# Kernel tuning notes

Measured on AMD Instinct MI355X. Metric: run time of the kernel, lower is better.

The kernel has to match this reference:

```python
import jax, jax.numpy as jnp
import numpy as np

DEPTH = 4  # default MLP(dim, depth=4) in NeuralMemory.__init__


def mlp_apply(W, x):
    # MLP.forward: x @ W0, then silu(x) @ Wi for i>0
    for i in range(DEPTH):
        if i:
            x = jax.nn.silu(x)
        x = x @ W[i]
    return x


def _loss(W, k, v):
    # default_loss_fn on a single token: (pred - target)^2 .mean(-1).sum() == mean over d
    pred = mlp_apply(W, k)
    return ((pred - v) ** 2).mean()


def setup_inputs() -> dict:
    key = jax.random.key(0)
    ks = jax.random.split(key, 6)
    b, n, d = 2, 1024, 128
    s = 1.0 / np.sqrt(d)  # scale weights for numerical sanity through the 4-layer chain
    return {
        "seq": jax.random.normal(ks[0], (b, n, d), dtype=jnp.float32),
        "W": jax.random.normal(ks[1], (DEPTH, d, d), dtype=jnp.float32) * s,
        "Wkv": jax.random.normal(ks[2], (d, 2 * d), dtype=jnp.float32) * s,
        "w_lr": jax.random.normal(ks[3], (d,), dtype=jnp.float32) * s,
        "w_mom": jax.random.normal(ks[4], (d,), dtype=jnp.float32) * s,
        "w_decay": jax.random.normal(ks[5], (d,), dtype=jnp.float32) * s,
    }


def reference(seq, W, Wkv, w_lr, w_mom, w_decay):
    # NeuralMemory.store_memories (past_memories=None)
    b, n, d = seq.shape
    adaptive_lr = seq @ w_lr                     # (b, n)  -- to_adaptive_step (no activation)
    adaptive_momentum = seq @ w_mom              # (b, n)  -- computed but unused in source snippet
    decay_factor = jax.nn.sigmoid(seq @ w_decay) # (b, n)  -- computed but unused in source snippet

    flat = seq.reshape(b * n, d)
    kv = flat @ Wkv
    keys, values = kv[:, :d], kv[:, d:]

    # per-sample grad_and_value over flattened tokens
    per_sample = jax.vmap(jax.value_and_grad(_loss), in_axes=(None, 0, 0))
    losses, grads = per_sample(W, keys, values)  # losses (b*n,), grads (b*n, DEPTH, d, d)

    grads = grads.reshape(b, n, DEPTH, d, d)
    grads = grads * (-adaptive_lr)[:, :, None, None, None]
    grads = jnp.cumsum(grads, axis=1)            # fast-weight cumulative updates

    next_memories = W[None] + grads[:, -1]       # (b, DEPTH, d, d)
    return grads, next_memories, losses.mean()
```

## Files before the change

kernel.cpp:

```cpp
#include <hip/hip_runtime.h>
#include <math.h>

#define D 128
#define NS 2048
#define NCHUNK 16
#define CLEN 64

__device__ __forceinline__ float sigmoidf_(float x) {
    return 1.0f / (1.0f + expf(-x));
}

__device__ __forceinline__ float matvec_col(const float* __restrict__ M,
                                            const float* x, int tid)
{
    float a0 = 0.f, a1 = 0.f, a2 = 0.f, a3 = 0.f;
#pragma unroll 4
    for (int r = 0; r < D; r += 4) {
        a0 += x[r]     * M[(r)     * D + tid];
        a1 += x[r + 1] * M[(r + 1) * D + tid];
        a2 += x[r + 2] * M[(r + 2) * D + tid];
        a3 += x[r + 3] * M[(r + 3) * D + tid];
    }
    return (a0 + a1) + (a2 + a3);
}

__global__ __launch_bounds__(256) void transposeW(
    const float* __restrict__ W, float* __restrict__ WT)
{
    const int l   = blockIdx.x >> 4;
    const int tl  = blockIdx.x & 15;
    const int tr  = tl >> 2, tc = tl & 3;
    const int tid = threadIdx.x;
    const int lr  = tid >> 5;
    const int lc  = tid & 31;
    __shared__ float tile[32][33];
#pragma unroll
    for (int k = 0; k < 4; ++k)
        tile[lr + 8 * k][lc] =
            W[l * 16384 + (tr * 32 + lr + 8 * k) * 128 + tc * 32 + lc];
    __syncthreads();
#pragma unroll
    for (int k = 0; k < 4; ++k)
        WT[l * 16384 + (tc * 32 + lr + 8 * k) * 128 + tr * 32 + lc] =
            tile[lc][lr + 8 * k];
}

__global__ __launch_bounds__(128) void phase1(
    const float* __restrict__ seq, const float* __restrict__ W,
    const float* __restrict__ WT, const float* __restrict__ Wkv,
    const float* __restrict__ w_lr,
    float* __restrict__ ws_u, float* __restrict__ ws_g,
    float* __restrict__ lossbuf)
{
    const int s   = blockIdx.x;
    const int tid = threadIdx.x;

    __shared__ float sseq[D], xbuf[D], vbuf[D], gbuf[D];
    __shared__ float red2[2];

    const float sv = seq[s * D + tid];
    sseq[tid] = sv;

    float p = sv * w_lr[tid];
#pragma unroll
    for (int off = 32; off > 0; off >>= 1) p += __shfl_down(p, off, 64);
    if ((tid & 63) == 0) red2[tid >> 6] = p;
    __syncthreads();
    const float scale = -(red2[0] + red2[1]);

    {
        float k0 = 0.f, k1 = 0.f, v0 = 0.f, v1 = 0.f;
#pragma unroll 4
        for (int r = 0; r < D; r += 2) {
            float x0 = sseq[r], x1 = sseq[r + 1];
            k0 += x0 * Wkv[r * 256 + tid];
            v0 += x0 * Wkv[r * 256 + 128 + tid];
            k1 += x1 * Wkv[(r + 1) * 256 + tid];
            v1 += x1 * Wkv[(r + 1) * 256 + 128 + tid];
        }
        float kacc = k0 + k1, vacc = v0 + v1;
        xbuf[tid] = kacc;
        vbuf[tid] = vacc;
        ws_u[(s * 4 + 0) * D + tid] = kacc;
    }
    __syncthreads();

    float h0r, h1r, h2r;
    {
        float h = matvec_col(W + 0 * 16384, xbuf, tid);
        h0r = h;
        float a = h * sigmoidf_(h);
        __syncthreads();
        xbuf[tid] = a;
        ws_u[(s * 4 + 1) * D + tid] = a;
        __syncthreads();
    }
    {
        float h = matvec_col(W + 1 * 16384, xbuf, tid);
        h1r = h;
        float a = h * sigmoidf_(h);
        __syncthreads();
        xbuf[tid] = a;
        ws_u[(s * 4 + 2) * D + tid] = a;
        __syncthreads();
    }
    {
        float h = matvec_col(W + 2 * 16384, xbuf, tid);
        h2r = h;
        float a = h * sigmoidf_(h);
        __syncthreads();
        xbuf[tid] = a;
        ws_u[(s * 4 + 3) * D + tid] = a;
        __syncthreads();
    }
    const float hfin = matvec_col(W + 3 * 16384, xbuf, tid);
    const float diff = hfin - vbuf[tid];

    {
        float lp = diff * diff;
#pragma unroll
        for (int off = 32; off > 0; off >>= 1) lp += __shfl_down(lp, off, 64);
        if ((tid & 63) == 0) red2[tid >> 6] = lp;
        __syncthreads();
        if (tid == 0) lossbuf[s] = (red2[0] + red2[1]) * (1.0f / 128.0f);
    }

    float g = diff * (2.0f / 128.0f);
    gbuf[tid] = g;
    ws_g[(s * 4 + 3) * D + tid] = scale * g;
    __syncthreads();

    {
        float da = matvec_col(WT + 3 * 16384, gbuf, tid);
        float sg = sigmoidf_(h2r);
        g = da * (sg * (1.0f + h2r * (1.0f - sg)));
    }
    __syncthreads();
    gbuf[tid] = g;
    ws_g[(s * 4 + 2) * D + tid] = scale * g;
    __syncthreads();

    {
        float da = matvec_col(WT + 2 * 16384, gbuf, tid);
        float sg = sigmoidf_(h1r);
        g = da * (sg * (1.0f + h1r * (1.0f - sg)));
    }
    __syncthreads();
    gbuf[tid] = g;
    ws_g[(s * 4 + 1) * D + tid] = scale * g;
    __syncthreads();

    {
        float da = matvec_col(WT + 1 * 16384, gbuf, tid);
        float sg = sigmoidf_(h0r);
        g = da * (sg * (1.0f + h0r * (1.0f - sg)));
    }
    ws_g[(s * 4 + 0) * D + tid] = scale * g;
}

__global__ __launch_bounds__(256) void phaseA(
    const float* __restrict__ ws_u, const float* __restrict__ ws_g,
    float* __restrict__ chunkS)
{
    const int bx    = blockIdx.x;
    const int half  = bx & 1;
    const int cs    = bx >> 1;
    const int j     = cs & 15;
    const int layer = (cs >> 4) & 3;
    const int b     = cs >> 6;
    const int tid   = threadIdx.x;
    const int hi    = tid >> 7;
    const int c     = tid & 127;

    __shared__ float us[2][64], gs[2][D];
    float acc[32];
#pragma unroll
    for (int k = 0; k < 32; ++k) acc[k] = 0.f;

    const int samp0 = b * 1024 + j * CLEN;
    float ru = 0.f, rg = 0.f;
    if (tid < 128) rg = ws_g[(samp0 * 4 + layer) * D + tid];
    if (tid < 64)  ru = ws_u[(samp0 * 4 + layer) * D + half * 64 + tid];

    for (int t = 0; t < CLEN; ++t) {
        const int pb = t & 1;
        if (tid < 128) gs[pb][tid] = rg;
        if (tid < 64)  us[pb][tid] = ru;
        if (t + 1 < CLEN) {
            const int samp = samp0 + t + 1;
            if (tid < 128) rg = ws_g[(samp * 4 + layer) * D + tid];
            if (tid < 64)  ru = ws_u[(samp * 4 + layer) * D + half * 64 + tid];
        }
        __syncthreads();
        const float gv = gs[pb][c];
#pragma unroll
        for (int k = 0; k < 32; ++k) acc[k] += us[pb][2 * k + hi] * gv;
    }
    float* out = chunkS + (size_t)cs * 16384 + half * 8192;
#pragma unroll
    for (int k = 0; k < 32; ++k) out[k * 256 + tid] = acc[k];
}

__global__ __launch_bounds__(256) void phaseA2(float* __restrict__ chunkS)
{
    const int g  = blockIdx.x * 256 + threadIdx.x;
    const int bl = g >> 14;
    const int e  = g & 16383;
    float* base = chunkS + (size_t)bl * NCHUNK * 16384 + e;
    float run = 0.f;
    for (int j = 0; j < NCHUNK; ++j) {
        float t = base[(size_t)j * 16384];
        base[(size_t)j * 16384] = run;
        run += t;
    }
}

__global__ __launch_bounds__(256) void phaseB(
    const float* __restrict__ ws_u, const float* __restrict__ ws_g,
    const float* __restrict__ chunkS, const float* __restrict__ W,
    float* __restrict__ out_grads, float* __restrict__ out_next)
{
    const int id    = blockIdx.x;
    const int rt    = id & 3;
    const int j     = (id >> 2) & 15;
    const int layer = (id >> 6) & 3;
    const int b     = id >> 8;
    const int cs    = (b * 4 + layer) * NCHUNK + j;
    const int tid   = threadIdx.x;

    const int c4 = (tid & 31) * 4;
    const int rq = tid >> 5;
    const int r0 = rt * 32 + rq * 4;

    float4 acc[4];
    const float* carry = chunkS + (size_t)cs * 16384;
#pragma unroll
    for (int k = 0; k < 4; ++k)
        acc[k] = *(const float4*)(carry + (r0 + k) * 128 + c4);

    const int samp0 = b * 1024 + j * CLEN;
    const float* gbase = ws_g + ((size_t)samp0 * 4 + layer) * D;
    const float* ubase = ws_u + ((size_t)samp0 * 4 + layer) * D;

    float4 gv = *(const float4*)(gbase + c4);
    float4 u4 = *(const float4*)(ubase + r0);

    for (int t = 0; t < CLEN; ++t) {
        float4 gn = gv, un = u4;
        if (t + 1 < CLEN) {
            gn = *(const float4*)(gbase + (t + 1) * 512 + c4);
            un = *(const float4*)(ubase + (t + 1) * 512 + r0);
        }
        float* obase = out_grads + ((size_t)(samp0 + t) * 4 + layer) * 16384;

        acc[0].x += u4.x * gv.x; acc[0].y += u4.x * gv.y;
        acc[0].z += u4.x * gv.z; acc[0].w += u4.x * gv.w;
        acc[1].x += u4.y * gv.x; acc[1].y += u4.y * gv.y;
        acc[1].z += u4.y * gv.z; acc[1].w += u4.y * gv.w;
        acc[2].x += u4.z * gv.x; acc[2].y += u4.z * gv.y;
        acc[2].z += u4.z * gv.z; acc[2].w += u4.z * gv.w;
        acc[3].x += u4.w * gv.x; acc[3].y += u4.w * gv.y;
        acc[3].z += u4.w * gv.z; acc[3].w += u4.w * gv.w;

        *(float4*)(obase + (r0 + 0) * 128 + c4) = acc[0];
        *(float4*)(obase + (r0 + 1) * 128 + c4) = acc[1];
        *(float4*)(obase + (r0 + 2) * 128 + c4) = acc[2];
        *(float4*)(obase + (r0 + 3) * 128 + c4) = acc[3];

        gv = gn; u4 = un;
    }

    if (j == NCHUNK - 1) {
#pragma unroll
        for (int k = 0; k < 4; ++k) {
            const int r = r0 + k;
            float4 w4 = *(const float4*)(W + layer * 16384 + r * 128 + c4);
            float4 o;
            o.x = acc[k].x + w4.x;
            o.y = acc[k].y + w4.y;
            o.z = acc[k].z + w4.z;
            o.w = acc[k].w + w4.w;
            *(float4*)(out_next + ((size_t)(b * 4 + layer)) * 16384 + r * 128 + c4) = o;
        }
    }
}

__global__ __launch_bounds__(256) void lossk(const float* __restrict__ lossbuf,
                                             float* __restrict__ out)
{
    __shared__ float red[256];
    const int tid = threadIdx.x;
    float s = 0.f;
    for (int i = tid; i < NS; i += 256) s += lossbuf[i];
    red[tid] = s;
    __syncthreads();
    for (int off = 128; off > 0; off >>= 1) {
        if (tid < off) red[tid] += red[tid + off];
        __syncthreads();
    }
    if (tid == 0) out[0] = red[0] * (1.0f / (float)NS);
}

extern "C" void kernel_launch(void* const* d_in, const int* in_sizes, int n_in,
                              void* d_out, int out_size, void* d_ws, size_t ws_size,
                              hipStream_t stream)
{
    const float* seq   = (const float*)d_in[0];
    const float* W     = (const float*)d_in[1];
    const float* Wkv   = (const float*)d_in[2];
    const float* w_lr  = (const float*)d_in[3];

    float* out = (float*)d_out;
    float* ws  = (float*)d_ws;

    float* ws_u    = ws;
    float* ws_g    = ws + 1048576;
    float* chunkS  = ws + 2097152;
    float* lossbuf = ws + 4194304;
    float* WT      = chunkS;

    float* out_grads = out;
    float* out_next  = out + 134217728;
    float* out_loss  = out + 134348800;

    transposeW<<<64, 256, 0, stream>>>(W, WT);
    phase1<<<NS, 128, 0, stream>>>(seq, W, WT, Wkv, w_lr, ws_u, ws_g, lossbuf);
    phaseA<<<256, 256, 0, stream>>>(ws_u, ws_g, chunkS);
    phaseA2<<<512, 256, 0, stream>>>(chunkS);
    phaseB<<<512, 256, 0, stream>>>(ws_u, ws_g, chunkS, W, out_grads, out_next);
    lossk<<<1, 256, 0, stream>>>(lossbuf, out_loss);
}
```

Measured before the change: 628.5 us.

## Batch four samples per matvec in phase1, finer chunking, nontemporal grad stores

phase1 now has each 128-thread group process four samples at once, so every weight element loaded from global memory is reused across four matvecs, and blocks hold 8 samples. The cumsum chunking doubles to 32 chunks of 32 when the workspace is large enough, giving phaseB 1024 blocks for more parallelism. The 512 MB gradient output is written with nontemporal stores to avoid polluting cache. Risks are higher register pressure in phase1 and a dependence on the available workspace size.

After: 624.8 us. Within noise of the previous version (-0.6%).

```diff
diff --git a/kernel.cpp b/kernel.cpp
--- a/kernel.cpp
+++ b/kernel.cpp
@@ -3,25 +3,33 @@
 
 #define D 128
 #define NS 2048
-#define NCHUNK 16
-#define CLEN 64
+
+typedef float v4f __attribute__((ext_vector_type(4)));
 
 __device__ __forceinline__ float sigmoidf_(float x) {
     return 1.0f / (1.0f + expf(-x));
 }
 
-__device__ __forceinline__ float matvec_col(const float* __restrict__ M,
-                                            const float* x, int tid)
-{
-    float a0 = 0.f, a1 = 0.f, a2 = 0.f, a3 = 0.f;
-#pragma unroll 4
+__device__ __forceinline__ void matvec4(const float* __restrict__ M,
+                                        const float (*xsg)[D], int lt,
+                                        float acc[4])
+{
+    acc[0] = 0.f; acc[1] = 0.f; acc[2] = 0.f; acc[3] = 0.f;
+#pragma unroll 2
     for (int r = 0; r < D; r += 4) {
-        a0 += x[r]     * M[(r)     * D + tid];
-        a1 += x[r + 1] * M[(r + 1) * D + tid];
-        a2 += x[r + 2] * M[(r + 2) * D + tid];
-        a3 += x[r + 3] * M[(r + 3) * D + tid];
-    }
-    return (a0 + a1) + (a2 + a3);
+        v4f x0 = *(const v4f*)&xsg[0][r];
+        v4f x1 = *(const v4f*)&xsg[1][r];
+        v4f x2 = *(const v4f*)&xsg[2][r];
+        v4f x3 = *(const v4f*)&xsg[3][r];
+#pragma unroll
+        for (int rr = 0; rr < 4; ++rr) {
+            float w = M[(r + rr) * D + lt];
+            acc[0] += x0[rr] * w;
+            acc[1] += x1[rr] * w;
+            acc[2] += x2[rr] * w;
+            acc[3] += x3[rr] * w;
+        }
+    }
 }
 
 __global__ __launch_bounds__(256) void transposeW(
@@ -45,119 +53,161 @@
             tile[lc][lr + 8 * k];
 }
 
-__global__ __launch_bounds__(128) void phase1(
+__global__ __launch_bounds__(256) void phase1(
     const float* __restrict__ seq, const float* __restrict__ W,
     const float* __restrict__ WT, const float* __restrict__ Wkv,
     const float* __restrict__ w_lr,
     float* __restrict__ ws_u, float* __restrict__ ws_g,
     float* __restrict__ lossbuf)
 {
-    const int s   = blockIdx.x;
     const int tid = threadIdx.x;
-
-    __shared__ float sseq[D], xbuf[D], vbuf[D], gbuf[D];
-    __shared__ float red2[2];
-
-    const float sv = seq[s * D + tid];
-    sseq[tid] = sv;
-
-    float p = sv * w_lr[tid];
-#pragma unroll
-    for (int off = 32; off > 0; off >>= 1) p += __shfl_down(p, off, 64);
-    if ((tid & 63) == 0) red2[tid >> 6] = p;
-    __syncthreads();
-    const float scale = -(red2[0] + red2[1]);
-
-    {
-        float k0 = 0.f, k1 = 0.f, v0 = 0.f, v1 = 0.f;
-#pragma unroll 4
-        for (int r = 0; r < D; r += 2) {
-            float x0 = sseq[r], x1 = sseq[r + 1];
-            k0 += x0 * Wkv[r * 256 + tid];
-            v0 += x0 * Wkv[r * 256 + 128 + tid];
-            k1 += x1 * Wkv[(r + 1) * 256 + tid];
-            v1 += x1 * Wkv[(r + 1) * 256 + 128 + tid];
-        }
-        float kacc = k0 + k1, vacc = v0 + v1;
-        xbuf[tid] = kacc;
-        vbuf[tid] = vacc;
-        ws_u[(s * 4 + 0) * D + tid] = kacc;
-    }
-    __syncthreads();
-
-    float h0r, h1r, h2r;
-    {
-        float h = matvec_col(W + 0 * 16384, xbuf, tid);
-        h0r = h;
-        float a = h * sigmoidf_(h);
-        __syncthreads();
-        xbuf[tid] = a;
-        ws_u[(s * 4 + 1) * D + tid] = a;
-        __syncthreads();
-    }
-    {
-        float h = matvec_col(W + 1 * 16384, xbuf, tid);
-        h1r = h;
-        float a = h * sigmoidf_(h);
-        __syncthreads();
-        xbuf[tid] = a;
-        ws_u[(s * 4 + 2) * D + tid] = a;
-        __syncthreads();
-    }
-    {
-        float h = matvec_col(W + 2 * 16384, xbuf, tid);
-        h2r = h;
-        float a = h * sigmoidf_(h);
-        __syncthreads();
-        xbuf[tid] = a;
-        ws_u[(s * 4 + 3) * D + tid] = a;
-        __syncthreads();
-    }
-    const float hfin = matvec_col(W + 3 * 16384, xbuf, tid);
-    const float diff = hfin - vbuf[tid];
-
-    {
-        float lp = diff * diff;
+    const int g   = tid >> 7;
+    const int lt  = tid & 127;
+    const int wv  = lt >> 6;
+    const int sbase = blockIdx.x * 8 + g * 4;
+
+    __shared__ float sseq[2][4][D];
+    __shared__ float xs[2][4][D];
+    __shared__ float red[2][4][2];
+
+#pragma unroll
+    for (int s = 0; s < 4; ++s)
+        sseq[g][s][lt] = seq[(sbase + s) * D + lt];
+
+    const float wlr = w_lr[lt];
+#pragma unroll
+    for (int s = 0; s < 4; ++s) {
+        float p = sseq[g][s][lt] * wlr;
+#pragma unroll
+        for (int off = 32; off > 0; off >>= 1) p += __shfl_down(p, off, 64);
+        if ((tid & 63) == 0) red[g][s][wv] = p;
+    }
+    __syncthreads();
+    float sc[4];
+#pragma unroll
+    for (int s = 0; s < 4; ++s) sc[s] = -(red[g][s][0] + red[g][s][1]);
+
+    float ka[4] = {0.f, 0.f, 0.f, 0.f}, va[4] = {0.f, 0.f, 0.f, 0.f};
+#pragma unroll 2
+    for (int r = 0; r < D; r += 4) {
+        v4f x0 = *(const v4f*)&sseq[g][0][r];
+        v4f x1 = *(const v4f*)&sseq[g][1][r];
+        v4f x2 = *(const v4f*)&sseq[g][2][r];
+        v4f x3 = *(const v4f*)&sseq[g][3][r];
+#pragma unroll
+        for (int rr = 0; rr < 4; ++rr) {
+            float wk  = Wkv[(r + rr) * 256 + lt];
+            float wv2 = Wkv[(r + rr) * 256 + 128 + lt];
+            ka[0] += x0[rr] * wk;  va[0] += x0[rr] * wv2;
+            ka[1] += x1[rr] * wk;  va[1] += x1[rr] * wv2;
+            ka[2] += x2[rr] * wk;  va[2] += x2[rr] * wv2;
+            ka[3] += x3[rr] * wk;  va[3] += x3[rr] * wv2;
+        }
+    }
+    float vr[4];
+#pragma unroll
+    for (int s = 0; s < 4; ++s) {
+        vr[s] = va[s];
+        xs[g][s][lt] = ka[s];
+        ws_u[((size_t)(sbase + s) * 4 + 0) * D + lt] = ka[s];
+    }
+    __syncthreads();
+
+    float h0r[4], h1r[4], h2r[4], acc[4];
+
+    matvec4(W + 0 * 16384, xs[g], lt, acc);
+    __syncthreads();
+#pragma unroll
+    for (int s = 0; s < 4; ++s) {
+        h0r[s] = acc[s];
+        float a = acc[s] * sigmoidf_(acc[s]);
+        xs[g][s][lt] = a;
+        ws_u[((size_t)(sbase + s) * 4 + 1) * D + lt] = a;
+    }
+    __syncthreads();
+
+    matvec4(W + 1 * 16384, xs[g], lt, acc);
+    __syncthreads();
+#pragma unroll
+    for (int s = 0; s < 4; ++s) {
+        h1r[s] = acc[s];
+        float a = acc[s] * sigmoidf_(acc[s]);
+        xs[g][s][lt] = a;
+        ws_u[((size_t)(sbase + s) * 4 + 2) * D + lt] = a;
+    }
+    __syncthreads();
+
+    matvec4(W + 2 * 16384, xs[g], lt, acc);
+    __syncthreads();
+#pragma unroll
+    for (int s = 0; s < 4; ++s) {
+        h2r[s] = acc[s];
+        float a = acc[s] * sigmoidf_(acc[s]);
+        xs[g][s][lt] = a;
+        ws_u[((size_t)(sbase + s) * 4 + 3) * D + lt] = a;
+    }
+    __syncthreads();
+
+    matvec4(W + 3 * 16384, xs[g], lt, acc);
+    float diff[4];
+#pragma unroll
+    for (int s = 0; s < 4; ++s) diff[s] = acc[s] - vr[s];
+
+#pragma unroll
+    for (int s = 0; s < 4; ++s) {
+        float lp = diff[s] * diff[s];
 #pragma unroll
         for (int off = 32; off > 0; off >>= 1) lp += __shfl_down(lp, off, 64);
-        if ((tid & 63) == 0) red2[tid >> 6] = lp;
-        __syncthreads();
-        if (tid == 0) lossbuf[s] = (red2[0] + red2[1]) * (1.0f / 128.0f);
-    }
-
-    float g = diff * (2.0f / 128.0f);
-    gbuf[tid] = g;
-    ws_g[(s * 4 + 3) * D + tid] = scale * g;
-    __syncthreads();
-
-    {
-        float da = matvec_col(WT + 3 * 16384, gbuf, tid);
-        float sg = sigmoidf_(h2r);
-        g = da * (sg * (1.0f + h2r * (1.0f - sg)));
-    }
-    __syncthreads();
-    gbuf[tid] = g;
-    ws_g[(s * 4 + 2) * D + tid] = scale * g;
-    __syncthreads();
-
-    {
-        float da = matvec_col(WT + 2 * 16384, gbuf, tid);
-        float sg = sigmoidf_(h1r);
-        g = da * (sg * (1.0f + h1r * (1.0f - sg)));
-    }
-    __syncthreads();
-    gbuf[tid] = g;
-    ws_g[(s * 4 + 1) * D + tid] = scale * g;
-    __syncthreads();
-
-    {
-        float da = matvec_col(WT + 1 * 16384, gbuf, tid);
-        float sg = sigmoidf_(h0r);
-        g = da * (sg * (1.0f + h0r * (1.0f - sg)));
-    }
-    ws_g[(s * 4 + 0) * D + tid] = scale * g;
-}
-
+        if ((tid & 63) == 0) red[g][s][wv] = lp;
+    }
+    __syncthreads();
+    if (lt == 0) {
+#pragma unroll
+        for (int s = 0; s < 4; ++s)
+            lossbuf[sbase + s] = (red[g][s][0] + red[g][s][1]) * (1.0f / 128.0f);
+    }
+
+    float gcur[4];
+#pragma unroll
+    for (int s = 0; s < 4; ++s) {
+        gcur[s] = diff[s] * (2.0f / 128.0f);
+        xs[g][s][lt] = gcur[s];
+        ws_g[((size_t)(sbase + s) * 4 + 3) * D + lt] = sc[s] * gcur[s];
+    }
+    __syncthreads();
+
+    matvec4(WT + 3 * 16384, xs[g], lt, acc);
+    __syncthreads();
+#pragma unroll
+    for (int s = 0; s < 4; ++s) {
+        float hv = h2r[s], sg = sigmoidf_(hv);
+        gcur[s] = acc[s] * (sg * (1.0f + hv * (1.0f - sg)));
+        xs[g][s][lt] = gcur[s];
+        ws_g[((size_t)(sbase + s) * 4 + 2) * D + lt] = sc[s] * gcur[s];
+    }
+    __syncthreads();
+
+    matvec4(WT + 2 * 16384, xs[g], lt, acc);
+    __syncthreads();
+#pragma unroll
+    for (int s = 0; s < 4; ++s) {
+        float hv = h1r[s], sg = sigmoidf_(hv);
+        gcur[s] = acc[s] * (sg * (1.0f + hv * (1.0f - sg)));
+        xs[g][s][lt] = gcur[s];
+        ws_g[((size_t)(sbase + s) * 4 + 1) * D + lt] = sc[s] * gcur[s];
+    }
+    __syncthreads();
+
+    matvec4(WT + 1 * 16384, xs[g], lt, acc);
+#pragma unroll
+    for (int s = 0; s < 4; ++s) {
+        float hv = h0r[s], sg = sigmoidf_(hv);
+        gcur[s] = acc[s] * (sg * (1.0f + hv * (1.0f - sg)));
+        ws_g[((size_t)(sbase + s) * 4 + 0) * D + lt] = sc[s] * gcur[s];
+    }
+}
+
+template<int NCH, int CL>
 __global__ __launch_bounds__(256) void phaseA(
     const float* __restrict__ ws_u, const float* __restrict__ ws_g,
     float* __restrict__ chunkS)
@@ -165,9 +215,9 @@
     const int bx    = blockIdx.x;
     const int half  = bx & 1;
     const int cs    = bx >> 1;
-    const int j     = cs & 15;
-    const int layer = (cs >> 4) & 3;
-    const int b     = cs >> 6;
+    const int j     = cs & (NCH - 1);
+    const int layer = (cs / NCH) & 3;
+    const int b     = cs / (NCH * 4);
     const int tid   = threadIdx.x;
     const int hi    = tid >> 7;
     const int c     = tid & 127;
@@ -177,16 +227,16 @@
 #pragma unroll
     for (int k = 0; k < 32; ++k) acc[k] = 0.f;
 
-    const int samp0 = b * 1024 + j * CLEN;
+    const int samp0 = b * 1024 + j * CL;
     float ru = 0.f, rg = 0.f;
     if (tid < 128) rg = ws_g[(samp0 * 4 + layer) * D + tid];
     if (tid < 64)  ru = ws_u[(samp0 * 4 + layer) * D + half * 64 + tid];
 
-    for (int t = 0; t < CLEN; ++t) {
+    for (int t = 0; t < CL; ++t) {
         const int pb = t & 1;
         if (tid < 128) gs[pb][tid] = rg;
         if (tid < 64)  us[pb][tid] = ru;
-        if (t + 1 < CLEN) {
+        if (t + 1 < CL) {
             const int samp = samp0 + t + 1;
             if (tid < 128) rg = ws_g[(samp * 4 + layer) * D + tid];
             if (tid < 64)  ru = ws_u[(samp * 4 + layer) * D + half * 64 + tid];
@@ -201,20 +251,22 @@
     for (int k = 0; k < 32; ++k) out[k * 256 + tid] = acc[k];
 }
 
+template<int NCH>
 __global__ __launch_bounds__(256) void phaseA2(float* __restrict__ chunkS)
 {
     const int g  = blockIdx.x * 256 + threadIdx.x;
     const int bl = g >> 14;
     const int e  = g & 16383;
-    float* base = chunkS + (size_t)bl * NCHUNK * 16384 + e;
+    float* base = chunkS + (size_t)bl * NCH * 16384 + e;
     float run = 0.f;
-    for (int j = 0; j < NCHUNK; ++j) {
+    for (int j = 0; j < NCH; ++j) {
         float t = base[(size_t)j * 16384];
         base[(size_t)j * 16384] = run;
         run += t;
     }
 }
 
+template<int NCH, int CL>
 __global__ __launch_bounds__(256) void phaseB(
     const float* __restrict__ ws_u, const float* __restrict__ ws_g,
     const float* __restrict__ chunkS, const float* __restrict__ W,
@@ -222,65 +274,59 @@
 {
     const int id    = blockIdx.x;
     const int rt    = id & 3;
-    const int j     = (id >> 2) & 15;
-    const int layer = (id >> 6) & 3;
-    const int b     = id >> 8;
-    const int cs    = (b * 4 + layer) * NCHUNK + j;
+    const int rest  = id >> 2;
+    const int j     = rest & (NCH - 1);
+    const int rest2 = rest / NCH;
+    const int layer = rest2 & 3;
+    const int b     = rest2 >> 2;
+    const int cs    = (b * 4 + layer) * NCH + j;
     const int tid   = threadIdx.x;
 
     const int c4 = (tid & 31) * 4;
     const int rq = tid >> 5;
     const int r0 = rt * 32 + rq * 4;
 
-    float4 acc[4];
+    v4f acc[4];
     const float* carry = chunkS + (size_t)cs * 16384;
 #pragma unroll
     for (int k = 0; k < 4; ++k)
-        acc[k] = *(const float4*)(carry + (r0 + k) * 128 + c4);
-
-    const int samp0 = b * 1024 + j * CLEN;
+        acc[k] = *(const v4f*)(carry + (r0 + k) * 128 + c4);
+
+    const int samp0 = b * 1024 + j * CL;
     const float* gbase = ws_g + ((size_t)samp0 * 4 + layer) * D;
     const float* ubase = ws_u + ((size_t)samp0 * 4 + layer) * D;
 
-    float4 gv = *(const float4*)(gbase + c4);
-    float4 u4 = *(const float4*)(ubase + r0);
-
-    for (int t = 0; t < CLEN; ++t) {
-        float4 gn = gv, un = u4;
-        if (t + 1 < CLEN) {
-            gn = *(const float4*)(gbase + (t + 1) * 512 + c4);
-            un = *(const float4*)(ubase + (t + 1) * 512 + r0);
+    v4f gv = *(const v4f*)(gbase + c4);
+    v4f u4 = *(const v4f*)(ubase + r0);
+
+    for (int t = 0; t < CL; ++t) {
+        v4f gn = gv, un = u4;
+        if (t + 1 < CL) {
+            gn = *(const v4f*)(gbase + (t + 1) * 512 + c4);
+            un = *(const v4f*)(ubase + (t + 1) * 512 + r0);
         }
         float* obase = out_grads + ((size_t)(samp0 + t) * 4 + layer) * 16384;
 
-        acc[0].x += u4.x * gv.x; acc[0].y += u4.x * gv.y;
-        acc[0].z += u4.x * gv.z; acc[0].w += u4.x * gv.w;
-        acc[1].x += u4.y * gv.x; acc[1].y += u4.y * gv.y;
-        acc[1].z += u4.y * gv.z; acc[1].w += u4.y * gv.w;
-        acc[2].x += u4.z * gv.x; acc[2].y += u4.z * gv.y;
-        acc[2].z += u4.z * gv.z; acc[2].w += u4.z * gv.w;
-        acc[3].x += u4.w * gv.x; acc[3].y += u4.w * gv.y;
-        acc[3].z += u4.w * gv.z; acc[3].w += u4.w * gv.w;
-
-        *(float4*)(obase + (r0 + 0) * 128 + c4) = acc[0];
-        *(float4*)(obase + (r0 + 1) * 128 + c4) = acc[1];
-        *(float4*)(obase + (r0 + 2) * 128 + c4) = acc[2];
-        *(float4*)(obase + (r0 + 3) * 128 + c4) = acc[3];
+        acc[0] += u4[0] * gv;
+        acc[1] += u4[1] * gv;
+        acc[2] += u4[2] * gv;
+        acc[3] += u4[3] * gv;
+
+        __builtin_nontemporal_store(acc[0], (v4f*)(obase + (r0 + 0) * 128 + c4));
+        __builtin_nontemporal_store(acc[1], (v4f*)(obase + (r0 + 1) * 128 + c4));
+        __builtin_nontemporal_store(acc[2], (v4f*)(obase + (r0 + 2) * 128 + c4));
+        __builtin_nontemporal_store(acc[3], (v4f*)(obase + (r0 + 3) * 128 + c4));
 
         gv = gn; u4 = un;
     }
 
-    if (j == NCHUNK - 1) {
+    if (j == NCH - 1) {
 #pragma unroll
         for (int k = 0; k < 4; ++k) {
             const int r = r0 + k;
-            float4 w4 = *(const float4*)(W + layer * 16384 + r * 128 + c4);
-            float4 o;
-            o.x = acc[k].x + w4.x;
-            o.y = acc[k].y + w4.y;
-            o.z = acc[k].z + w4.z;
-            o.w = acc[k].w + w4.w;
-            *(float4*)(out_next + ((size_t)(b * 4 + layer)) * 16384 + r * 128 + c4) = o;
+            v4f w4 = *(const v4f*)(W + layer * 16384 + r * 128 + c4);
+            v4f o = acc[k] + w4;
+            *(v4f*)(out_next + ((size_t)(b * 4 + layer)) * 16384 + r * 128 + c4) = o;
         }
     }
 }
@@ -313,10 +359,14 @@
     float* out = (float*)d_out;
     float* ws  = (float*)d_ws;
 
+    const size_t need32 = ((size_t)2097152 + (size_t)8 * 32 * 16384 + 2048) * 4;
+    const bool big = ws_size >= need32;
+    const size_t chunkFloats = (size_t)8 * (big ? 32 : 16) * 16384;
+
     float* ws_u    = ws;
     float* ws_g    = ws + 1048576;
     float* chunkS  = ws + 2097152;
-    float* lossbuf = ws + 4194304;
+    float* lossbuf = ws + 2097152 + chunkFloats;
     float* WT      = chunkS;
 
     float* out_grads = out;
@@ -324,9 +374,17 @@
     float* out_loss  = out + 134348800;
 
     transposeW<<<64, 256, 0, stream>>>(W, WT);
-    phase1<<<NS, 128, 0, stream>>>(seq, W, WT, Wkv, w_lr, ws_u, ws_g, lossbuf);
-    phaseA<<<256, 256, 0, stream>>>(ws_u, ws_g, chunkS);
-    phaseA2<<<512, 256, 0, stream>>>(chunkS);
-    phaseB<<<512, 256, 0, stream>>>(ws_u, ws_g, chunkS, W, out_grads, out_next);
+    phase1<<<NS / 8, 256, 0, stream>>>(seq, W, WT, Wkv, w_lr, ws_u, ws_g, lossbuf);
+    if (big) {
+        phaseA<32, 32><<<512, 256, 0, stream>>>(ws_u, ws_g, chunkS);
+        phaseA2<32><<<512, 256, 0, stream>>>(chunkS);
+        phaseB<32, 32><<<1024, 256, 0, stream>>>(ws_u, ws_g, chunkS, W,
+                                                 out_grads, out_next);
+    } else {
+        phaseA<16, 64><<<256, 256, 0, stream>>>(ws_u, ws_g, chunkS);
+        phaseA2<16><<<512, 256, 0, stream>>>(chunkS);
+        phaseB<16, 64><<<512, 256, 0, stream>>>(ws_u, ws_g, chunkS, W,
+                                                out_grads, out_next);
+    }
     lossk<<<1, 256, 0, stream>>>(lossbuf, out_loss);
 }
```
